# Optimization experiments

Measured on AMD Instinct MI355X. Metric: run time of the kernel, lower is better.

## Reference

```python
import jax, jax.numpy as jnp
import numpy as np

B, D_IN, D_H = 4096, 1024, 1024  # cell_dim == hidden_dim required by the elementwise math


def _lin(x, W, b):
    # torch nn.Linear: y = x @ W.T + b, W: [out, in]
    return x @ W.T + b


def setup_inputs() -> dict:
    key = jax.random.key(0)
    ks = jax.random.split(key, 20)
    s2 = 1.0 / np.sqrt(D_IN + D_H)
    s1 = 1.0 / np.sqrt(D_IN)
    inp = {
        "input_tensor": jax.random.normal(ks[0], (B, D_IN), jnp.float32),
        "h_cur": jax.random.uniform(ks[1], (B, D_H), jnp.float32),
        "excited_cell": jax.random.uniform(ks[2], (B, D_H), jnp.float32),
        "time_cell": jax.random.uniform(ks[3], (B, D_H), jnp.float32),
        "Wt_w": jax.random.normal(ks[4], (D_H, D_IN + D_H), jnp.float32) * s2,
        "Wt_b": jax.random.normal(ks[5], (D_H,), jnp.float32) * s2,
        "Wa_w": jax.random.normal(ks[6], (D_H, D_IN + D_H), jnp.float32) * s2,
        "Wa_b": jax.random.normal(ks[7], (D_H,), jnp.float32) * s2,
        "Eh_w": jax.random.normal(ks[8], (D_H, D_IN + D_H), jnp.float32) * s2,
        "Eh_b": jax.random.normal(ks[9], (D_H,), jnp.float32) * s2,
        "Hw_w": jax.random.normal(ks[10], (D_H, D_IN + D_H), jnp.float32) * s2,
        "Hw_b": jax.random.normal(ks[11], (D_H,), jnp.float32) * s2,
        "Tr_w": jax.random.normal(ks[12], (D_H, D_IN), jnp.float32) * s1,
        "Tr_b": jax.random.normal(ks[13], (D_H,), jnp.float32) * s1,
        "Ei_w": jax.random.normal(ks[14], (D_H, D_IN), jnp.float32) * s1,
        "Ei_b": jax.random.normal(ks[15], (D_H,), jnp.float32) * s1,
    }
    return inp


def reference(input_tensor, h_cur, excited_cell, time_cell,
              Wt_w, Wt_b, Wa_w, Wa_b, Eh_w, Eh_b, Hw_w, Hw_b,
              Tr_w, Tr_b, Ei_w, Ei_b):
    combined = jnp.concatenate([input_tensor, h_cur], axis=1)  # [B, D_IN+D_H]
    energy_init = jax.nn.sigmoid(_lin(input_tensor, Ei_w, Ei_b))
    ratio = jax.nn.sigmoid(_lin(input_tensor, Tr_w, Tr_b))
    up_time = jnp.tanh(_lin(combined, Wt_w, Wt_b))
    time_cell = ratio * jax.nn.relu(time_cell + up_time) - 1.0
    leap = (time_cell <= 0).astype(jnp.float32)
    time_cell = (1.0 - leap) * time_cell
    energy = leap * excited_cell
    excited_cell = excited_cell - energy + energy_init * (1.0 - leap)
    absorb_energy = jax.nn.sigmoid(_lin(combined, Wa_w, Wa_b))
    excited_cell = excited_cell + absorb_energy
    h_up = h_cur * energy
    h_state = jnp.tanh(_lin(jnp.concatenate([input_tensor, h_up], axis=1), Eh_w, Eh_b))
    h_weight = jax.nn.sigmoid(_lin(combined, Hw_w, Hw_b))
    h_next = jnp.tanh((1.0 - h_weight) * h_cur + h_weight * h_state)
    return (h_next, excited_cell, time_cell)
```

## Files before the change

kernel.cpp:

```cpp
#include <hip/hip_runtime.h>
#include <math.h>


typedef __attribute__((ext_vector_type(4))) float f32x4;
typedef __attribute__((ext_vector_type(8))) _Float16 half8;
typedef __attribute__((ext_vector_type(4))) _Float16 half4;

#define NEL (4096 * 1024)
#define DELTA 3.0e-3f
#define CAP 1300000

__device__ __forceinline__ float sigm(float x) { return 1.0f / (1.0f + expf(-x)); }

__device__ __forceinline__ void gload16(const void* g, void* l) {
  __builtin_amdgcn_global_load_lds(
      (const __attribute__((address_space(1))) void*)g,
      (__attribute__((address_space(3))) void*)l, 16, 0, 0);
}

template <int OP>
__device__ __forceinline__ void gemm_body(
    _Float16* sm, const int brow, const int bcol,
    const _Float16* A1h, const _Float16* A2h,
    const _Float16* Wh, const float* bias, const int K,
    float* outF, _Float16* outH, const _Float16* hw_p, const float* hc_p)
{
  _Float16* As = sm;
  _Float16* Bs = sm + 8192;
  const int tid = threadIdx.x;
  const int lane = tid & 63;
  const int w = tid >> 6;
  const int wr = w >> 1, wc = w & 1;
  const int lr = lane & 15, lq = lane >> 4;

  f32x4 acc[4][4] = {};

  for (int k0 = 0; k0 < K; k0 += 64) {
    const _Float16* Ah = (k0 < 1024) ? A1h : A2h;
    const int kk = k0 & 1023;
    __syncthreads();
#pragma unroll
    for (int i = 0; i < 4; ++i) {
      const int c_lin = i * 256 + tid;
      const int row = c_lin >> 3;
      const int c = c_lin & 7;
      const int src = (c ^ (row & 7)) * 8;
      gload16(Ah + (size_t)(brow + row) * 1024 + kk + src, &As[row * 64 + c * 8]);
      gload16(Wh + (size_t)(bcol + row) * K + k0 + src,    &Bs[row * 64 + c * 8]);
    }
    __syncthreads();

#pragma unroll
    for (int h = 0; h < 2; ++h) {
      half8 a[4], b[4];
#pragma unroll
      for (int m = 0; m < 4; ++m) {
        const int row = wr * 64 + m * 16 + lr;
        const int ch = (lq + 4 * h) ^ (row & 7);
        a[m] = *(const half8*)&As[row * 64 + ch * 8];
      }
#pragma unroll
      for (int n = 0; n < 4; ++n) {
        const int row = wc * 64 + n * 16 + lr;
        const int ch = (lq + 4 * h) ^ (row & 7);
        b[n] = *(const half8*)&Bs[row * 64 + ch * 8];
      }
#pragma unroll
      for (int m = 0; m < 4; ++m)
#pragma unroll
        for (int n = 0; n < 4; ++n)
          acc[m][n] = __builtin_amdgcn_mfma_f32_16x16x32_f16(a[m], b[n], acc[m][n], 0, 0, 0);
    }
  }

  float bv[4];
#pragma unroll
  for (int n = 0; n < 4; ++n) bv[n] = bias[bcol + wc * 64 + n * 16 + lr];

#pragma unroll
  for (int m = 0; m < 4; ++m)
#pragma unroll
    for (int n = 0; n < 4; ++n) {
      const int col = bcol + wc * 64 + n * 16 + lr;
#pragma unroll
      for (int j = 0; j < 4; ++j) {
        const int rowg = brow + wr * 64 + m * 16 + lq * 4 + j;
        const size_t idx = (size_t)rowg * 1024 + col;
        const float v = acc[m][n][j] + bv[n];
        if (OP == 0)      outF[idx] = sigm(v);
        else if (OP == 1) outF[idx] = tanhf(v);
        else if (OP == 2) outH[idx] = (_Float16)sigm(v);
        else {
          const float hs = tanhf(v);
          const float hwv = (float)hw_p[idx];
          const float hcv = hc_p[idx];
          outF[idx] = tanhf((1.0f - hwv) * hcv + hwv * hs);
        }
      }
    }
}

__global__ __launch_bounds__(256, 3)
void qurnn_gemm5(const _Float16* inpH, const _Float16* hcH,
                 const _Float16* WtH, const float* Wt_b,
                 const _Float16* WaH, const float* Wa_b,
                 const _Float16* HwH, const float* Hw_b,
                 const _Float16* TrH, const float* Tr_b,
                 const _Float16* EiH, const float* Ei_b,
                 float* ws_ut, _Float16* ws_ab, _Float16* ws_hw,
                 float* out_tm, _Float16* ws_ei)
{
  __shared__ __align__(16) _Float16 sm[2 * 8192];
  const int brow = (blockIdx.x & 31) * 128;
  const int bcol = (blockIdx.x >> 5) * 128;
  switch (blockIdx.z) {
    case 0: gemm_body<1>(sm, brow, bcol, inpH, hcH, WtH, Wt_b, 2048, ws_ut, nullptr, nullptr, nullptr); break;
    case 1: gemm_body<2>(sm, brow, bcol, inpH, hcH, WaH, Wa_b, 2048, nullptr, ws_ab, nullptr, nullptr); break;
    case 2: gemm_body<2>(sm, brow, bcol, inpH, hcH, HwH, Hw_b, 2048, nullptr, ws_hw, nullptr, nullptr); break;
    case 3: gemm_body<0>(sm, brow, bcol, inpH, nullptr, TrH, Tr_b, 1024, out_tm, nullptr, nullptr, nullptr); break;
    default:gemm_body<2>(sm, brow, bcol, inpH, nullptr, EiH, Ei_b, 1024, nullptr, ws_ei, nullptr, nullptr); break;
  }
}

__global__ __launch_bounds__(256, 3)
void qurnn_eh(const _Float16* inpH, const _Float16* hup,
              const _Float16* EhH, const float* Eh_b,
              const _Float16* hw, const float* hcur, float* out_h)
{
  __shared__ __align__(16) _Float16 sm[2 * 8192];
  const int brow = (blockIdx.x & 31) * 128;
  const int bcol = (blockIdx.x >> 5) * 128;
  gemm_body<3>(sm, brow, bcol, inpH, hup, EhH, Eh_b, 2048,
               out_h, nullptr, hw, hcur);
}

__global__ __launch_bounds__(256)
void qurnn_cell(const f32x4* tc, const f32x4* ec, const f32x4* hc,
                const f32x4* ut, const half4* ab, const half4* ei,
                f32x4* out_ex, f32x4* out_tm, half4* hup,
                int* count, int* list)
{
  __shared__ int l_cnt, l_base;
  __shared__ int l_idx[1024];
  if (threadIdx.x == 0) l_cnt = 0;
  __syncthreads();

  const int i = blockIdx.x * 256 + threadIdx.x;
  const f32x4 tcv = tc[i], ecv = ec[i], hcv = hc[i];
  const f32x4 rav = out_tm[i];
  const f32x4 utv = ut[i];
  const half4 abv = ab[i], eiv = ei[i];
  f32x4 to, eo; half4 ho;
#pragma unroll
  for (int j = 0; j < 4; ++j) {
    const float t = rav[j] * fmaxf(tcv[j] + utv[j], 0.0f) - 1.0f;
    const bool leap = (t <= 0.0f);
    to[j] = leap ? 0.0f : t;
    eo[j] = (leap ? 0.0f : ecv[j] + (float)eiv[j]) + (float)abv[j];
    ho[j] = (_Float16)(leap ? hcv[j] * ecv[j] : 0.0f);
    if (fabsf(t) < DELTA) {
      const int p = atomicAdd(&l_cnt, 1);
      l_idx[p] = i * 4 + j;
    }
  }
  out_tm[i] = to;
  out_ex[i] = eo;
  hup[i] = ho;

  __syncthreads();
  if (threadIdx.x == 0 && l_cnt > 0) l_base = atomicAdd(count, l_cnt);
  __syncthreads();
  for (int e = threadIdx.x; e < l_cnt; e += 256) {
    const int pos = l_base + e;
    if (pos < CAP) list[pos] = l_idx[e];
  }
}

__global__ __launch_bounds__(256)
void qurnn_fixup(const int* count, const int* list,
                 const float* inp, const float* hcur,
                 const float* Tr_w, const float* Tr_b,
                 const float* Wt_w, const float* Wt_b,
                 const _Float16* ei, const _Float16* ab,
                 const float* tc, const float* ec,
                 float* out_tm, float* out_ex, _Float16* hup)
{
  const int gtid = blockIdx.x * 256 + threadIdx.x;
  const int wid = gtid >> 6, lane = gtid & 63;
  const int nw = gridDim.x * 4;
  const int n = min(*count, CAP);
  for (int e = wid; e < n; e += nw) {
    const int idx = list[e];
    const int row = idx >> 10, col = idx & 1023;
    const f32x4* irow = (const f32x4*)(inp  + (size_t)row * 1024);
    const f32x4* hrow = (const f32x4*)(hcur + (size_t)row * 1024);
    const f32x4* trw  = (const f32x4*)(Tr_w + (size_t)col * 1024);
    const f32x4* wtw  = (const f32x4*)(Wt_w + (size_t)col * 2048);
    float dTr = 0.0f, dWt = 0.0f;
#pragma unroll
    for (int k = 0; k < 4; ++k) {
      const int q = k * 64 + lane;
      const f32x4 a = irow[q], h = hrow[q];
      const f32x4 w1 = trw[q], w2 = wtw[q], w3 = wtw[256 + q];
#pragma unroll
      for (int j = 0; j < 4; ++j) {
        dTr = fmaf(a[j], w1[j], dTr);
        dWt = fmaf(a[j], w2[j], dWt);
        dWt = fmaf(h[j], w3[j], dWt);
      }
    }
#pragma unroll
    for (int s = 32; s; s >>= 1) {
      dTr += __shfl_xor(dTr, s);
      dWt += __shfl_xor(dWt, s);
    }
    if (lane == 0) {
      const float ratio = sigm(dTr + Tr_b[col]);
      const float utv = tanhf(dWt + Wt_b[col]);
      const float t = ratio * fmaxf(tc[idx] + utv, 0.0f) - 1.0f;
      const bool leap = (t <= 0.0f);
      out_tm[idx] = leap ? 0.0f : t;
      out_ex[idx] = (leap ? 0.0f : ec[idx] + (float)ei[idx]) + (float)ab[idx];
      hup[idx] = (_Float16)(leap ? hcur[idx] * ec[idx] : 0.0f);
    }
  }
}

__global__ __launch_bounds__(256)
void convert_k(const float* inp, const float* hcur,
               const float* Wt_w, const float* Tr_w, const float* Wa_w,
               const float* Hw_w, const float* Eh_w, const float* Ei_w,
               _Float16* inpH, _Float16* hcH, _Float16* WtH, _Float16* TrH,
               _Float16* WaH, _Float16* HwH, _Float16* EhH, _Float16* EiH,
               int* count)
{
  if (blockIdx.z == 0 && blockIdx.x == 0 && threadIdx.x == 0) *count = 0;
  const float* src; _Float16* dh; int n4;
  switch (blockIdx.z) {
    case 0: src = inp;  dh = inpH; n4 = NEL / 4;           break;
    case 1: src = hcur; dh = hcH;  n4 = NEL / 4;           break;
    case 2: src = Wt_w; dh = WtH;  n4 = (1024 * 2048) / 4; break;
    case 3: src = Tr_w; dh = TrH;  n4 = (1024 * 1024) / 4; break;
    case 4: src = Wa_w; dh = WaH;  n4 = (1024 * 2048) / 4; break;
    case 5: src = Hw_w; dh = HwH;  n4 = (1024 * 2048) / 4; break;
    case 6: src = Eh_w; dh = EhH;  n4 = (1024 * 2048) / 4; break;
    default:src = Ei_w; dh = EiH;  n4 = (1024 * 1024) / 4; break;
  }
  for (int i = blockIdx.x * 256 + threadIdx.x; i < n4; i += gridDim.x * 256) {
    const f32x4 v = ((const f32x4*)src)[i];
    half4 h;
#pragma unroll
    for (int j = 0; j < 4; ++j) h[j] = (_Float16)v[j];
    ((half4*)dh)[i] = h;
  }
}

extern "C" void kernel_launch(void* const* d_in, const int* in_sizes, int n_in,
                              void* d_out, int out_size, void* d_ws, size_t ws_size,
                              hipStream_t stream)
{
  const float* inp  = (const float*)d_in[0];
  const float* hcur = (const float*)d_in[1];
  const float* ec   = (const float*)d_in[2];
  const float* tc   = (const float*)d_in[3];
  const float* Wt_w = (const float*)d_in[4];
  const float* Wt_b = (const float*)d_in[5];
  const float* Wa_w = (const float*)d_in[6];
  const float* Wa_b = (const float*)d_in[7];
  const float* Eh_w = (const float*)d_in[8];
  const float* Eh_b = (const float*)d_in[9];
  const float* Hw_w = (const float*)d_in[10];
  const float* Hw_b = (const float*)d_in[11];
  const float* Tr_w = (const float*)d_in[12];
  const float* Tr_b = (const float*)d_in[13];
  const float* Ei_w = (const float*)d_in[14];
  const float* Ei_b = (const float*)d_in[15];

  float* out_h  = (float*)d_out;
  float* out_ex = out_h + NEL;
  float* out_tm = out_ex + NEL;

  char* wsb = (char*)d_ws;
  float*    ws_ut  = (float*)(wsb);
  _Float16* ws_ab  = (_Float16*)(wsb + (16u << 20));
  _Float16* ws_ei  = (_Float16*)(wsb + (24u << 20));
  _Float16* ws_hup = (_Float16*)(wsb + (32u << 20));
  _Float16* ws_hw  = (_Float16*)(wsb + (40u << 20));
  _Float16* inpH   = (_Float16*)(wsb + (48u << 20));
  _Float16* hcH    = (_Float16*)(wsb + (56u << 20));
  _Float16* WtH    = (_Float16*)(wsb + (64u << 20));
  _Float16* TrH    = (_Float16*)(wsb + (68u << 20));
  _Float16* WaH    = (_Float16*)(wsb + (70u << 20));
  _Float16* HwH    = (_Float16*)(wsb + (74u << 20));
  _Float16* EhH    = (_Float16*)(wsb + (78u << 20));
  _Float16* EiH    = (_Float16*)(wsb + (82u << 20));
  int*      d_cnt  = (int*)(wsb + (84u << 20));
  int*      d_list = (int*)(wsb + (84u << 20) + 256);

  convert_k<<<dim3(512, 1, 8), 256, 0, stream>>>(
      inp, hcur, Wt_w, Tr_w, Wa_w, Hw_w, Eh_w, Ei_w,
      inpH, hcH, WtH, TrH, WaH, HwH, EhH, EiH, d_cnt);

  qurnn_gemm5<<<dim3(256, 1, 5), 256, 0, stream>>>(
      inpH, hcH, WtH, Wt_b, WaH, Wa_b, HwH, Hw_b, TrH, Tr_b, EiH, Ei_b,
      ws_ut, ws_ab, ws_hw, out_tm, ws_ei);

  qurnn_cell<<<dim3(4096), 256, 0, stream>>>(
      (const f32x4*)tc, (const f32x4*)ec, (const f32x4*)hcur,
      (const f32x4*)ws_ut, (const half4*)ws_ab, (const half4*)ws_ei,
      (f32x4*)out_ex, (f32x4*)out_tm, (half4*)ws_hup, d_cnt, d_list);

  qurnn_fixup<<<dim3(1024), 256, 0, stream>>>(
      d_cnt, d_list, inp, hcur, Tr_w, Tr_b, Wt_w, Wt_b,
      ws_ei, ws_ab, tc, ec, out_tm, out_ex, ws_hup);

  qurnn_eh<<<dim3(256), 256, 0, stream>>>(
      inpH, ws_hup, EhH, Eh_b, ws_hw, hcur, out_h);
}
```

Measured before the change: 210.6 us.

## Bucket fixup candidates per column and interleave GEMM groups in the grid

The near-threshold candidate list becomes per-column buckets built with global atomics, so each fixup block handles one column and stages that column's Tr/Wt weight rows in shared memory instead of rereading them from global memory for every element. The five-GEMM launch is also flattened so the five weight groups are interleaved across block IDs, which may balance the mix of K=2048 and K=1024 work across CUs. The per-column cap of 256 entries silently drops candidates if a column overflows, and the global atomics on 1024 counters may contend more than the old block-local aggregation.

```diff
diff --git a/kernel.cpp b/kernel.cpp
--- a/kernel.cpp
+++ b/kernel.cpp
@@ -8,7 +8,7 @@
 
 #define NEL (4096 * 1024)
 #define DELTA 3.0e-3f
-#define CAP 1300000
+#define COLCAP 256
 
 __device__ __forceinline__ float sigm(float x) { return 1.0f / (1.0f + expf(-x)); }
 
@@ -111,9 +111,11 @@
                  float* out_tm, _Float16* ws_ei)
 {
   __shared__ __align__(16) _Float16 sm[2 * 8192];
-  const int brow = (blockIdx.x & 31) * 128;
-  const int bcol = (blockIdx.x >> 5) * 128;
-  switch (blockIdx.z) {
+  const int g = blockIdx.x % 5;
+  const int tile = blockIdx.x / 5;
+  const int brow = (tile & 31) * 128;
+  const int bcol = (tile >> 5) * 128;
+  switch (g) {
     case 0: gemm_body<1>(sm, brow, bcol, inpH, hcH, WtH, Wt_b, 2048, ws_ut, nullptr, nullptr, nullptr); break;
     case 1: gemm_body<2>(sm, brow, bcol, inpH, hcH, WaH, Wa_b, 2048, nullptr, ws_ab, nullptr, nullptr); break;
     case 2: gemm_body<2>(sm, brow, bcol, inpH, hcH, HwH, Hw_b, 2048, nullptr, ws_hw, nullptr, nullptr); break;
@@ -138,13 +140,8 @@
 void qurnn_cell(const f32x4* tc, const f32x4* ec, const f32x4* hc,
                 const f32x4* ut, const half4* ab, const half4* ei,
                 f32x4* out_ex, f32x4* out_tm, half4* hup,
-                int* count, int* list)
-{
-  __shared__ int l_cnt, l_base;
-  __shared__ int l_idx[1024];
-  if (threadIdx.x == 0) l_cnt = 0;
-  __syncthreads();
-
+                int* colcnt, int* collist)
+{
   const int i = blockIdx.x * 256 + threadIdx.x;
   const f32x4 tcv = tc[i], ecv = ec[i], hcv = hc[i];
   const f32x4 rav = out_tm[i];
@@ -159,25 +156,19 @@
     eo[j] = (leap ? 0.0f : ecv[j] + (float)eiv[j]) + (float)abv[j];
     ho[j] = (_Float16)(leap ? hcv[j] * ecv[j] : 0.0f);
     if (fabsf(t) < DELTA) {
-      const int p = atomicAdd(&l_cnt, 1);
-      l_idx[p] = i * 4 + j;
+      const int e = i * 4 + j;
+      const int col = e & 1023;
+      const int p = atomicAdd(&colcnt[col], 1);
+      if (p < COLCAP) collist[col * COLCAP + p] = e >> 10;
     }
   }
   out_tm[i] = to;
   out_ex[i] = eo;
   hup[i] = ho;
-
-  __syncthreads();
-  if (threadIdx.x == 0 && l_cnt > 0) l_base = atomicAdd(count, l_cnt);
-  __syncthreads();
-  for (int e = threadIdx.x; e < l_cnt; e += 256) {
-    const int pos = l_base + e;
-    if (pos < CAP) list[pos] = l_idx[e];
-  }
 }
 
 __global__ __launch_bounds__(256)
-void qurnn_fixup(const int* count, const int* list,
+void qurnn_fixup(const int* colcnt, const int* collist,
                  const float* inp, const float* hcur,
                  const float* Tr_w, const float* Tr_b,
                  const float* Wt_w, const float* Wt_b,
@@ -185,23 +176,30 @@
                  const float* tc, const float* ec,
                  float* out_tm, float* out_ex, _Float16* hup)
 {
-  const int gtid = blockIdx.x * 256 + threadIdx.x;
-  const int wid = gtid >> 6, lane = gtid & 63;
-  const int nw = gridDim.x * 4;
-  const int n = min(*count, CAP);
-  for (int e = wid; e < n; e += nw) {
-    const int idx = list[e];
-    const int row = idx >> 10, col = idx & 1023;
+  const int col = blockIdx.x;
+  const int n_c = min(colcnt[col], COLCAP);
+  if (n_c == 0) return;
+  __shared__ float wTr[1024];
+  __shared__ float wWt[2048];
+  const int tid = threadIdx.x;
+  for (int k = tid; k < 1024; k += 256) wTr[k] = Tr_w[(size_t)col * 1024 + k];
+  for (int k = tid; k < 2048; k += 256) wWt[k] = Wt_w[(size_t)col * 2048 + k];
+  __syncthreads();
+
+  const int wid = tid >> 6, lane = tid & 63;
+  for (int e = wid; e < n_c; e += 4) {
+    const int row = collist[col * COLCAP + e];
+    const int idx = row * 1024 + col;
     const f32x4* irow = (const f32x4*)(inp  + (size_t)row * 1024);
     const f32x4* hrow = (const f32x4*)(hcur + (size_t)row * 1024);
-    const f32x4* trw  = (const f32x4*)(Tr_w + (size_t)col * 1024);
-    const f32x4* wtw  = (const f32x4*)(Wt_w + (size_t)col * 2048);
     float dTr = 0.0f, dWt = 0.0f;
 #pragma unroll
     for (int k = 0; k < 4; ++k) {
       const int q = k * 64 + lane;
       const f32x4 a = irow[q], h = hrow[q];
-      const f32x4 w1 = trw[q], w2 = wtw[q], w3 = wtw[256 + q];
+      const f32x4 w1 = *(const f32x4*)&wTr[q * 4];
+      const f32x4 w2 = *(const f32x4*)&wWt[q * 4];
+      const f32x4 w3 = *(const f32x4*)&wWt[1024 + q * 4];
 #pragma unroll
       for (int j = 0; j < 4; ++j) {
         dTr = fmaf(a[j], w1[j], dTr);
@@ -232,9 +230,11 @@
                const float* Hw_w, const float* Eh_w, const float* Ei_w,
                _Float16* inpH, _Float16* hcH, _Float16* WtH, _Float16* TrH,
                _Float16* WaH, _Float16* HwH, _Float16* EhH, _Float16* EiH,
-               int* count)
-{
-  if (blockIdx.z == 0 && blockIdx.x == 0 && threadIdx.x == 0) *count = 0;
+               int* colcnt)
+{
+  if (blockIdx.z == 0 && blockIdx.x == 0) {
+    for (int k = threadIdx.x; k < 1024; k += 256) colcnt[k] = 0;
+  }
   const float* src; _Float16* dh; int n4;
   switch (blockIdx.z) {
     case 0: src = inp;  dh = inpH; n4 = NEL / 4;           break;
@@ -294,24 +294,24 @@
   _Float16* HwH    = (_Float16*)(wsb + (74u << 20));
   _Float16* EhH    = (_Float16*)(wsb + (78u << 20));
   _Float16* EiH    = (_Float16*)(wsb + (82u << 20));
-  int*      d_cnt  = (int*)(wsb + (84u << 20));
-  int*      d_list = (int*)(wsb + (84u << 20) + 256);
+  int*      d_ccnt = (int*)(wsb + (84u << 20));
+  int*      d_clst = (int*)(wsb + (84u << 20) + 4096);
 
   convert_k<<<dim3(512, 1, 8), 256, 0, stream>>>(
       inp, hcur, Wt_w, Tr_w, Wa_w, Hw_w, Eh_w, Ei_w,
-      inpH, hcH, WtH, TrH, WaH, HwH, EhH, EiH, d_cnt);
-
-  qurnn_gemm5<<<dim3(256, 1, 5), 256, 0, stream>>>(
+      inpH, hcH, WtH, TrH, WaH, HwH, EhH, EiH, d_ccnt);
+
+  qurnn_gemm5<<<dim3(1280), 256, 0, stream>>>(
       inpH, hcH, WtH, Wt_b, WaH, Wa_b, HwH, Hw_b, TrH, Tr_b, EiH, Ei_b,
       ws_ut, ws_ab, ws_hw, out_tm, ws_ei);
 
   qurnn_cell<<<dim3(4096), 256, 0, stream>>>(
       (const f32x4*)tc, (const f32x4*)ec, (const f32x4*)hcur,
       (const f32x4*)ws_ut, (const half4*)ws_ab, (const half4*)ws_ei,
-      (f32x4*)out_ex, (f32x4*)out_tm, (half4*)ws_hup, d_cnt, d_list);
+      (f32x4*)out_ex, (f32x4*)out_tm, (half4*)ws_hup, d_ccnt, d_clst);
 
   qurnn_fixup<<<dim3(1024), 256, 0, stream>>>(
-      d_cnt, d_list, inp, hcur, Tr_w, Tr_b, Wt_w, Wt_b,
+      d_ccnt, d_clst, inp, hcur, Tr_w, Tr_b, Wt_w, Wt_b,
       ws_ei, ws_ab, tc, ec, out_tm, out_ex, ws_hup);
 
   qurnn_eh<<<dim3(256), 256, 0, stream>>>(
```

New measurement: 219.6 us. 1.04x slower.
